# Kernel optimization log

Hardware: AMD Instinct MI355X
Metric: run time of the kernel (lower is better)

The kernel has to match this reference:

```python
import jax, jax.numpy as jnp
import numpy as np

D_MODEL = 1024
N_HEADS = 16
N_EXPERTS = 8
TOP_K = 2
EXPERT_HIDDEN = D_MODEL * 4 // N_EXPERTS  # 512, per MoELayer default


def layer_norm(x, g, b, eps=1e-5):
    mu = jnp.mean(x, axis=-1, keepdims=True)
    var = jnp.var(x, axis=-1, keepdims=True)
    return (x - mu) * jax.lax.rsqrt(var + eps) * g + b


def setup_inputs() -> dict:
    key = jax.random.key(0)
    ks = jax.random.split(key, 12)
    s = 1.0 / np.sqrt(D_MODEL)
    return {
        "x": jax.random.normal(ks[0], (2, 2048, D_MODEL), dtype=jnp.float32),
        "Wq": jax.random.normal(ks[1], (D_MODEL, D_MODEL), dtype=jnp.float32) * s,
        "Wk": jax.random.normal(ks[2], (D_MODEL, D_MODEL), dtype=jnp.float32) * s,
        "Wv": jax.random.normal(ks[3], (D_MODEL, D_MODEL), dtype=jnp.float32) * s,
        "Wo": jax.random.normal(ks[4], (D_MODEL, D_MODEL), dtype=jnp.float32) * s,
        "g1": jnp.ones((D_MODEL,), jnp.float32),
        "b1": jnp.zeros((D_MODEL,), jnp.float32),
        "g2": jnp.ones((D_MODEL,), jnp.float32),
        "b2": jnp.zeros((D_MODEL,), jnp.float32),
        "Wg": jax.random.normal(ks[5], (D_MODEL, N_EXPERTS), dtype=jnp.float32) * s,
        "W1": jax.random.normal(ks[6], (N_EXPERTS, D_MODEL, EXPERT_HIDDEN), dtype=jnp.float32) * s,
        "W2": jax.random.normal(ks[7], (N_EXPERTS, EXPERT_HIDDEN, D_MODEL), dtype=jnp.float32) * (1.0 / np.sqrt(EXPERT_HIDDEN)),
    }


def reference(x, Wq, Wk, Wv, Wo, g1, b1, g2, b2, Wg, W1, W2):
    B, S, D = x.shape
    H, dk = N_HEADS, D // N_HEADS

    # ---- pre-norm attention + residual (dropout = identity in eval) ----
    xn = layer_norm(x, g1, b1)
    q = (xn @ Wq).reshape(B, S, H, dk).transpose(0, 2, 1, 3)  # [B,H,S,dk]
    k = (xn @ Wk).reshape(B, S, H, dk).transpose(0, 2, 1, 3)
    v = (xn @ Wv).reshape(B, S, H, dk).transpose(0, 2, 1, 3)
    scores = jnp.einsum("bhqd,bhkd->bhqk", q, k) / np.sqrt(dk)
    attn = jax.nn.softmax(scores, axis=-1)
    o = jnp.einsum("bhqk,bhkd->bhqd", attn, v)
    o = o.transpose(0, 2, 1, 3).reshape(B, S, D) @ Wo
    x = x + o

    # ---- pre-norm MoE + residual ----
    xn2 = layer_norm(x, g2, b2)
    xf = xn2.reshape(B * S, D)  # [T, D]
    gate = xf @ Wg  # [T, E]
    topv, topi = jax.lax.top_k(gate, TOP_K)  # [T, K]
    probs = jax.nn.softmax(topv, axis=-1)    # softmax over top-k scores
    # dense combine weights [T, E] (top-k indices are distinct)
    cw = jnp.sum(jax.nn.one_hot(topi, N_EXPERTS, dtype=xf.dtype) * probs[..., None], axis=1)
    h = jax.nn.relu(jnp.einsum("td,edh->teh", xf, W1))  # [T,E,Hid]
    y = jnp.einsum("teh,ehd->ted", h, W2)               # [T,E,D]
    moe = jnp.einsum("ted,te->td", y, cw).reshape(B, S, D)
    return x + moe
```

## Files before the change

### kernel.cpp

```cpp
#include <hip/hip_runtime.h>

typedef __attribute__((ext_vector_type(8))) _Float16 f16x8;
typedef __attribute__((ext_vector_type(4))) _Float16 f16x4;
typedef __attribute__((ext_vector_type(8))) short bf16x8;
typedef __attribute__((ext_vector_type(4))) float f32x4;
typedef __attribute__((ext_vector_type(4))) unsigned short u16x4;
typedef __attribute__((ext_vector_type(4))) float fx4;

#define D_MODEL 1024
#define N_HEADS 16
#define SEQ 2048
#define TOKENS 4096
#define N_EXP 8
#define EHID 512
#define LO_S 2048.0f
#define INV_LO (1.0f / 2048.0f)
#define QSCALE 0.18033688011112043f
#define DTHR 11.0f

__device__ inline unsigned short f2bf(float f) {
  union { float f; unsigned u; } v; v.f = f;
  unsigned u = v.u;
  return (unsigned short)((u + 0x7FFFu + ((u >> 16) & 1u)) >> 16);
}

__device__ inline void split16(float v, _Float16& h, _Float16& l) {
  h = (_Float16)v;
  l = (_Float16)((v - (float)h) * LO_S);
}

__device__ inline void gload_lds16(const void* g, void* lds) {
  __builtin_amdgcn_global_load_lds((const __attribute__((address_space(1))) void*)g,
                                   (__attribute__((address_space(3))) void*)lds, 16, 0, 0);
}

__global__ __launch_bounds__(256) void ln_f16s_kernel(const float* __restrict__ x, const float* __restrict__ g,
                                                      const float* __restrict__ b,
                                                      _Float16* __restrict__ xh, _Float16* __restrict__ xl) {
  int t = blockIdx.x, tid = threadIdx.x;
  const float* row = x + (size_t)t * D_MODEL;
  fx4 v = *(const fx4*)(row + tid * 4);
  float s = v[0] + v[1] + v[2] + v[3];
  float s2 = v[0]*v[0] + v[1]*v[1] + v[2]*v[2] + v[3]*v[3];
  #pragma unroll
  for (int off = 1; off < 64; off <<= 1) { s += __shfl_xor(s, off); s2 += __shfl_xor(s2, off); }
  __shared__ float red[8];
  int wv = tid >> 6, wl = tid & 63;
  if (wl == 0) { red[wv] = s; red[4 + wv] = s2; }
  __syncthreads();
  s = red[0] + red[1] + red[2] + red[3];
  s2 = red[4] + red[5] + red[6] + red[7];
  float mu = s * (1.f / 1024.f);
  float var = s2 * (1.f / 1024.f) - mu * mu;
  float rstd = rsqrtf(var + 1e-5f);
  int kk = tid * 4;
  f16x4 oh, ol;
  #pragma unroll
  for (int c = 0; c < 4; c++) {
    float y = (v[c] - mu) * rstd * g[kk + c] + b[kk + c];
    _Float16 h, lo; split16(y, h, lo);
    oh[c] = h; ol[c] = lo;
  }
  *(f16x4*)(xh + (size_t)t * D_MODEL + kk) = oh;
  *(f16x4*)(xl + (size_t)t * D_MODEL + kk) = ol;
}

__global__ __launch_bounds__(256) void tcast4_kernel(const float* __restrict__ s0, const float* __restrict__ s1,
                                                     const float* __restrict__ s2, const float* __restrict__ s3,
                                                     _Float16* __restrict__ qkvh, _Float16* __restrict__ qkvl,
                                                     _Float16* __restrict__ woh, _Float16* __restrict__ wol) {
  int z = blockIdx.z;
  const float* src = (z == 0) ? s0 : (z == 1) ? s1 : (z == 2) ? s2 : s3;
  _Float16* dh = (z < 3) ? qkvh + (size_t)z * 1048576 : woh;
  _Float16* dl = (z < 3) ? qkvl + (size_t)z * 1048576 : wol;
  __shared__ float tile[32][33];
  int c0 = blockIdx.x * 32, r0 = blockIdx.y * 32;
  int tx = threadIdx.x & 31, ty = threadIdx.x >> 5;
  #pragma unroll
  for (int i = 0; i < 4; i++) tile[ty + 8*i][tx] = src[(size_t)(r0 + ty + 8*i) * 1024 + c0 + tx];
  __syncthreads();
  #pragma unroll
  for (int i = 0; i < 4; i++) {
    float v = tile[tx][ty + 8*i];
    _Float16 h, lo; split16(v, h, lo);
    size_t idx = (size_t)(c0 + ty + 8*i) * 1024 + r0 + tx;
    dh[idx] = h; dl[idx] = lo;
  }
}

__global__ __launch_bounds__(256) void tcast_bf16_kernel(const float* __restrict__ src, unsigned short* __restrict__ dst,
                                                         int R, int C) {
  __shared__ float tile[32][33];
  size_t mo = (size_t)blockIdx.z * R * C;
  src += mo; dst += mo;
  int c0 = blockIdx.x * 32, r0 = blockIdx.y * 32;
  int tx = threadIdx.x & 31, ty = threadIdx.x >> 5;
  #pragma unroll
  for (int i = 0; i < 4; i++) tile[ty + 8*i][tx] = src[(size_t)(r0 + ty + 8*i) * C + c0 + tx];
  __syncthreads();
  #pragma unroll
  for (int i = 0; i < 4; i++) dst[(size_t)(c0 + ty + 8*i) * R + r0 + tx] = f2bf(tile[tx][ty + 8*i]);
}

__device__ inline void gemm128s(const _Float16* __restrict__ Ah, const _Float16* __restrict__ Al,
                                const _Float16* __restrict__ Bh, const _Float16* __restrict__ Bl,
                                int lda, int ldb, int K, int bm, int bn,
                                _Float16* lsbuf, f32x4 (&acc)[4][4], f32x4 (&accx)[4][4]) {
  const int tid = threadIdx.x, w = tid >> 6, l = tid & 63, lr = l & 15, lg = l >> 4;
  const int wr = (w >> 1) * 64, wc = (w & 1) * 64;
  int ca = (((tid & 3) ^ ((tid >> 3) & 3)) * 8);
  int ra0 = tid >> 2, ra1 = 64 + (tid >> 2);
  const _Float16* gA0 = Ah + (size_t)(bm + ra0) * lda + ca;
  const _Float16* gA1 = Ah + (size_t)(bm + ra1) * lda + ca;
  const _Float16* gA2 = Al + (size_t)(bm + ra0) * lda + ca;
  const _Float16* gA3 = Al + (size_t)(bm + ra1) * lda + ca;
  const _Float16* gB0 = Bh + (size_t)(bn + ra0) * ldb + ca;
  const _Float16* gB1 = Bh + (size_t)(bn + ra1) * ldb + ca;
  const _Float16* gB2 = Bl + (size_t)(bn + ra0) * ldb + ca;
  const _Float16* gB3 = Bl + (size_t)(bn + ra1) * ldb + ca;
  char* base = (char*)lsbuf;
  const int wo = w * 1024;
#define STAGE8(bb, ko) do { \
    gload_lds16(gA0 + (ko), (bb) + wo);         gload_lds16(gA1 + (ko), (bb) + 4096 + wo);  \
    gload_lds16(gA2 + (ko), (bb) + 8192 + wo);  gload_lds16(gA3 + (ko), (bb) + 12288 + wo); \
    gload_lds16(gB0 + (ko), (bb) + 16384 + wo); gload_lds16(gB1 + (ko), (bb) + 20480 + wo); \
    gload_lds16(gB2 + (ko), (bb) + 24576 + wo); gload_lds16(gB3 + (ko), (bb) + 28672 + wo); } while (0)
  STAGE8(base, 0);
  __syncthreads();
  const int swzB = ((lg ^ ((lr >> 1) & 3)) << 4);
  int cur = 0;
  for (int ko = 0; ko < K; ko += 32) {
    char* bR = base + cur * 32768;
    if (ko + 32 < K) STAGE8(base + (cur ^ 1) * 32768, ko + 32);
    f16x8 ah[4], al4[4], bh4[4], bl4[4];
    #pragma unroll
    for (int m = 0; m < 4; m++) {
      int roff = (wr + m * 16 + lr) * 64 + swzB;
      ah[m]  = *(const f16x8*)(bR + roff);
      al4[m] = *(const f16x8*)(bR + 8192 + roff);
    }
    #pragma unroll
    for (int n = 0; n < 4; n++) {
      int roff = (wc + n * 16 + lr) * 64 + swzB;
      bh4[n] = *(const f16x8*)(bR + 16384 + roff);
      bl4[n] = *(const f16x8*)(bR + 24576 + roff);
    }
    __builtin_amdgcn_s_setprio(1);
    #pragma unroll
    for (int m = 0; m < 4; m++)
      #pragma unroll
      for (int n = 0; n < 4; n++) {
        acc[m][n]  = __builtin_amdgcn_mfma_f32_16x16x32_f16(ah[m], bh4[n], acc[m][n], 0, 0, 0);
        accx[m][n] = __builtin_amdgcn_mfma_f32_16x16x32_f16(ah[m], bl4[n], accx[m][n], 0, 0, 0);
        accx[m][n] = __builtin_amdgcn_mfma_f32_16x16x32_f16(al4[m], bh4[n], accx[m][n], 0, 0, 0);
      }
    __builtin_amdgcn_s_setprio(0);
    __syncthreads();
    cur ^= 1;
  }
#undef STAGE8
}

__global__ __launch_bounds__(256) void gemm_qkv_kernel(const _Float16* __restrict__ xh, const _Float16* __restrict__ xl,
                                                       const _Float16* __restrict__ Wh, const _Float16* __restrict__ Wl,
                                                       _Float16* __restrict__ qh, _Float16* __restrict__ ql,
                                                       _Float16* __restrict__ kh, _Float16* __restrict__ kl,
                                                       _Float16* __restrict__ vh, _Float16* __restrict__ vl) {
  __shared__ _Float16 ls[32768];
  f32x4 acc[4][4] = {}, accx[4][4] = {};
  int bid = blockIdx.x;
  int sw = (bid & 7) * 96 + (bid >> 3);
  int bm = (sw & 31) * 128, bn = (sw >> 5) * 128;
  gemm128s(xh, xl, Wh, Wl, 1024, 1024, 1024, bm, bn, ls, acc, accx);
  const int tid = threadIdx.x, w = tid >> 6, l = tid & 63, lr = l & 15, lg = l >> 4;
  const int wr = (w >> 1) * 64, wc = (w & 1) * 64;
  #pragma unroll
  for (int m = 0; m < 4; m++) {
    int row0 = bm + wr + m * 16 + lg * 4;
    #pragma unroll
    for (int n = 0; n < 4; n++) {
      int col = bn + wc + n * 16 + lr;
      int mat = col >> 10;
      int c = col & 1023, h = c >> 6, d = c & 63;
      if (mat == 2) {
        int bb = row0 >> 11, ss = row0 & 2047;
        int tile = ss >> 5, kvs = ss & 31;
        f16x4 ph, pl;
        #pragma unroll
        for (int j = 0; j < 4; j++) {
          float v = acc[m][n][j] + accx[m][n][j] * INV_LO;
          _Float16 hh, ll; split16(v, hh, ll);
          ph[j] = hh; pl[j] = ll;
        }
        size_t base = ((size_t)(bb * N_HEADS + h) * 64 + tile) * 2048;
        int off = d * 32 + ((((kvs >> 3) ^ ((d >> 1) & 3)) << 3) | (kvs & 7));
        *(f16x4*)(vh + base + off) = ph;
        *(f16x4*)(vl + base + off) = pl;
      } else if (mat == 1) {
        #pragma unroll
        for (int j = 0; j < 4; j++) {
          float v = acc[m][n][j] + accx[m][n][j] * INV_LO;
          _Float16 hh, ll; split16(v, hh, ll);
          int t = row0 + j, bb = t >> 11, ss = t & 2047;
          int tile = ss >> 5, r = ss & 31;
          size_t base = ((size_t)(bb * N_HEADS + h) * 64 + tile) * 2048;
          int off = r * 64 + ((((d >> 3) ^ (r & 7)) << 3) | (d & 7));
          kh[base + off] = hh; kl[base + off] = ll;
        }
      } else {
        #pragma unroll
        for (int j = 0; j < 4; j++) {
          float v = (acc[m][n][j] + accx[m][n][j] * INV_LO) * QSCALE;
          _Float16 hh, ll; split16(v, hh, ll);
          int t = row0 + j, bb = t >> 11, ss = t & 2047;
          size_t idx = ((size_t)(bb * N_HEADS + h) * SEQ + ss) * 64 + d;
          qh[idx] = hh; ql[idx] = ll;
        }
      }
    }
  }
}

__global__ __launch_bounds__(256, 4) void flash_kernel(const _Float16* __restrict__ qhp, const _Float16* __restrict__ qlp,
                                                       const _Float16* __restrict__ khs, const _Float16* __restrict__ kls,
                                                       const _Float16* __restrict__ vhs, const _Float16* __restrict__ vls,
                                                       _Float16* __restrict__ oh, _Float16* __restrict__ ol) {
  __shared__ _Float16 lsKV[2][8192];
  __shared__ _Float16 lsP[4][2][512];
  int wgid = blockIdx.x;
  int xcd = wgid & 7, kk = wgid >> 3;
  int bh = xcd * 4 + (kk >> 5), qt = kk & 31;
  int tid = threadIdx.x, w = tid >> 6, l = tid & 63, lr = l & 15, lg = l >> 4;
  int q0 = qt * 64 + w * 16;
  const _Float16* qhb = qhp + (size_t)bh * SEQ * 64;
  const _Float16* qlb = qlp + (size_t)bh * SEQ * 64;
  f16x8 qfh[2], qfl[2];
  #pragma unroll
  for (int ks = 0; ks < 2; ks++) {
    size_t idx = (size_t)(q0 + lr) * 64 + ks * 32 + lg * 8;
    qfh[ks] = *(const f16x8*)(qhb + idx);
    qfl[ks] = *(const f16x8*)(qlb + idx);
  }
  const _Float16* splane = (w == 0) ? khs : (w == 1) ? kls : (w == 2) ? vhs : vls;
  const _Float16* sbase = splane + (size_t)bh * 131072 + l * 8;

  f32x4 acc[4] = {}, accx[4] = {};
  float mst = -1e30f, lst = 0.f;

  {
    const _Float16* sp = sbase;
    _Float16* dd = &lsKV[0][w * 2048];
    gload_lds16(sp, dd); gload_lds16(sp + 512, dd + 512);
    gload_lds16(sp + 1024, dd + 1024); gload_lds16(sp + 1536, dd + 1536);
  }
  __syncthreads();

  for (int t = 0; t < 64; t++) {
    int bR = t & 1;
    if (t < 63) {
      const _Float16* sp = sbase + (size_t)(t + 1) * 2048;
      _Float16* dd = &lsKV[bR ^ 1][w * 2048];
      gload_lds16(sp, dd); gload_lds16(sp + 512, dd + 512);
      gload_lds16(sp + 1024, dd + 1024); gload_lds16(sp + 1536, dd + 1536);
    }
    char* bufB = (char*)&lsKV[bR][0];

    f32x4 s[2] = {}, sx[2] = {};
    #pragma unroll
    for (int ks = 0; ks < 2; ks++) {
      f16x8 kfh[2], kfl[2];
      #pragma unroll
      for (int m = 0; m < 2; m++) {
        int off = (m * 16 + lr) * 128 + (((ks * 4 + lg) ^ (lr & 7)) << 4);
        kfh[m] = *(const f16x8*)(bufB + off);
        kfl[m] = *(const f16x8*)(bufB + 4096 + off);
      }
      __builtin_amdgcn_s_setprio(1);
      #pragma unroll
      for (int m = 0; m < 2; m++) {
        s[m]  = __builtin_amdgcn_mfma_f32_16x16x32_f16(kfh[m], qfh[ks], s[m], 0, 0, 0);
        sx[m] = __builtin_amdgcn_mfma_f32_16x16x32_f16(kfh[m], qfl[ks], sx[m], 0, 0, 0);
        sx[m] = __builtin_amdgcn_mfma_f32_16x16x32_f16(kfl[m], qfh[ks], sx[m], 0, 0, 0);
      }
      __builtin_amdgcn_s_setprio(0);
    }

    float tm = -3e38f;
    #pragma unroll
    for (int m = 0; m < 2; m++)
      #pragma unroll
      for (int j = 0; j < 4; j++) {
        s[m][j] += sx[m][j] * INV_LO;
        tm = fmaxf(tm, s[m][j]);
      }
    tm = fmaxf(tm, __shfl_xor(tm, 16));
    tm = fmaxf(tm, __shfl_xor(tm, 32));
    if (!__all(tm - mst <= DTHR)) {
      float mnew = fmaxf(mst, tm);
      float corr = exp2f(mst - mnew);
      #pragma unroll
      for (int m2 = 0; m2 < 4; m2++)
        #pragma unroll
        for (int j = 0; j < 4; j++) { acc[m2][j] *= corr; accx[m2][j] *= corr; }
      lst *= corr;
      mst = mnew;
    }
    float psum = 0.f;
    #pragma unroll
    for (int m = 0; m < 2; m++) {
      f16x4 ph, pl;
      #pragma unroll
      for (int j = 0; j < 4; j++) {
        float p = exp2f(s[m][j] - mst);
        psum += p;
        _Float16 hh, ll; split16(p, hh, ll);
        ph[j] = hh; pl[j] = ll;
      }
      int boff = lr * 64 + ((((m * 2 + (lg >> 1)) ^ ((lr >> 1) & 3)) << 4) | ((lg & 1) * 8));
      *(f16x4*)((char*)&lsP[w][0][0] + boff) = ph;
      *(f16x4*)((char*)&lsP[w][1][0] + boff) = pl;
    }
    psum += __shfl_xor(psum, 16);
    psum += __shfl_xor(psum, 32);
    lst += psum;

    int poff = lr * 64 + ((lg ^ ((lr >> 1) & 3)) << 4);
    f16x8 pfh = *(const f16x8*)((char*)&lsP[w][0][0] + poff);
    f16x8 pfl = *(const f16x8*)((char*)&lsP[w][1][0] + poff);
    __builtin_amdgcn_s_setprio(1);
    #pragma unroll
    for (int m2 = 0; m2 < 4; m2++) {
      int voff = (m2 * 16 + lr) * 64 + ((lg ^ ((lr >> 1) & 3)) << 4);
      f16x8 vfh = *(const f16x8*)(bufB + 8192 + voff);
      f16x8 vfl = *(const f16x8*)(bufB + 12288 + voff);
      acc[m2]  = __builtin_amdgcn_mfma_f32_16x16x32_f16(vfh, pfh, acc[m2], 0, 0, 0);
      accx[m2] = __builtin_amdgcn_mfma_f32_16x16x32_f16(vfh, pfl, accx[m2], 0, 0, 0);
      accx[m2] = __builtin_amdgcn_mfma_f32_16x16x32_f16(vfl, pfh, accx[m2], 0, 0, 0);
    }
    __builtin_amdgcn_s_setprio(0);
    __syncthreads();
  }

  float inv = 1.f / lst;
  int b = bh >> 4, h = bh & 15;
  int tkn = b * SEQ + q0 + lr;
  #pragma unroll
  for (int m2 = 0; m2 < 4; m2++) {
    f16x4 ph, pl;
    #pragma unroll
    for (int j = 0; j < 4; j++) {
      float o = (acc[m2][j] + accx[m2][j] * INV_LO) * inv;
      _Float16 hh, ll; split16(o, hh, ll);
      ph[j] = hh; pl[j] = ll;
    }
    size_t idx = (size_t)tkn * D_MODEL + h * 64 + m2 * 16 + lg * 4;
    *(f16x4*)(oh + idx) = ph;
    *(f16x4*)(ol + idx) = pl;
  }
}

__global__ __launch_bounds__(256) void gemm_oproj_kernel(const _Float16* __restrict__ ah, const _Float16* __restrict__ al,
                                                         const _Float16* __restrict__ Wh, const _Float16* __restrict__ Wl,
                                                         const float* __restrict__ x, float* __restrict__ out) {
  __shared__ _Float16 ls[32768];
  f32x4 acc[4][4] = {}, accx[4][4] = {};
  int bid = blockIdx.x;
  int sw = (bid & 7) * 32 + (bid >> 3);
  int bm = (sw & 31) * 128, bn = (sw >> 5) * 128;
  gemm128s(ah, al, Wh, Wl, 1024, 1024, 1024, bm, bn, ls, acc, accx);
  const int tid = threadIdx.x, w = tid >> 6, l = tid & 63, lr = l & 15, lg = l >> 4;
  const int wr = (w >> 1) * 64, wc = (w & 1) * 64;
  #pragma unroll
  for (int m = 0; m < 4; m++) {
    int row0 = bm + wr + m * 16 + lg * 4;
    #pragma unroll
    for (int n = 0; n < 4; n++) {
      int col = bn + wc + n * 16 + lr;
      #pragma unroll
      for (int j = 0; j < 4; j++) {
        size_t idx = (size_t)(row0 + j) * D_MODEL + col;
        out[idx] = (acc[m][n][j] + accx[m][n][j] * INV_LO) + x[idx];
      }
    }
  }
}

__global__ __launch_bounds__(256) void gate_kernel(const float* __restrict__ x1, const float* __restrict__ Wg,
                                                   const float* __restrict__ g2, const float* __restrict__ b2,
                                                   unsigned short* __restrict__ xn2,
                                                   int* __restrict__ cnt, int* __restrict__ topi,
                                                   float* __restrict__ topw) {
  int t = blockIdx.x * 4 + (threadIdx.x >> 6);
  int l = threadIdx.x & 63;
  const float* row = x1 + (size_t)t * D_MODEL;
  fx4 v[4];
  float s = 0.f, s2 = 0.f;
  #pragma unroll
  for (int i = 0; i < 4; i++) {
    v[i] = *(const fx4*)(row + l * 16 + i * 4);
    #pragma unroll
    for (int c = 0; c < 4; c++) { s += v[i][c]; s2 += v[i][c] * v[i][c]; }
  }
  #pragma unroll
  for (int off = 1; off < 64; off <<= 1) { s += __shfl_xor(s, off); s2 += __shfl_xor(s2, off); }
  float mu = s * (1.f / 1024.f);
  float var = s2 * (1.f / 1024.f) - mu * mu;
  float rstd = rsqrtf(var + 1e-5f);
  float a8[8] = {0,0,0,0,0,0,0,0};
  #pragma unroll
  for (int i = 0; i < 4; i++) {
    u16x4 ox;
    #pragma unroll
    for (int c = 0; c < 4; c++) {
      int kk = l * 16 + i * 4 + c;
      float xv = (v[i][c] - mu) * rstd * g2[kk] + b2[kk];
      ox[c] = f2bf(xv);
      const float* wr_ = Wg + (size_t)kk * 8;
      fx4 wa = *(const fx4*)wr_;
      fx4 wb = *(const fx4*)(wr_ + 4);
      a8[0] += xv * wa[0]; a8[1] += xv * wa[1]; a8[2] += xv * wa[2]; a8[3] += xv * wa[3];
      a8[4] += xv * wb[0]; a8[5] += xv * wb[1]; a8[6] += xv * wb[2]; a8[7] += xv * wb[3];
    }
    *(u16x4*)(xn2 + (size_t)t * D_MODEL + l * 16 + i * 4) = ox;
  }
  #pragma unroll
  for (int e = 0; e < 8; e++)
    #pragma unroll
    for (int off = 1; off < 64; off <<= 1) a8[e] += __shfl_xor(a8[e], off);
  if (l == 0) {
    int i0 = 0; float v0 = a8[0];
    #pragma unroll
    for (int e = 1; e < 8; e++) if (a8[e] > v0) { v0 = a8[e]; i0 = e; }
    int i1 = -1; float v1 = -3.4e38f;
    #pragma unroll
    for (int e = 0; e < 8; e++) if (e != i0 && a8[e] > v1) { v1 = a8[e]; i1 = e; }
    float p0 = 1.f / (1.f + __expf(v1 - v0));
    topi[t * 2] = i0; topi[t * 2 + 1] = i1;
    topw[t * 2] = p0; topw[t * 2 + 1] = 1.f - p0;
    atomicAdd(&cnt[i0], 1); atomicAdd(&cnt[i1], 1);
  }
}

__global__ void init_kernel(int* cnt, int* perm) {
  int i = blockIdx.x * 256 + threadIdx.x;
  if (i < 8) cnt[i] = 0;
  if (i < 8448) perm[i] = 0;
}

__global__ void offsets_kernel(const int* __restrict__ cnt, int* __restrict__ poff) {
  if (threadIdx.x == 0) {
    int a = 0;
    for (int e = 0; e < 8; e++) { poff[e] = a; a += ((cnt[e] + 31) >> 5) << 5; }
  }
}

__global__ __launch_bounds__(256) void scatter_kernel(const int* __restrict__ topi,
                                                      const int* __restrict__ poff, int* __restrict__ perm,
                                                      int* __restrict__ slot_of) {
  int e = blockIdx.x, tid = threadIdx.x;
  __shared__ int basesh;
  __shared__ int wsum[4];
  if (tid == 0) basesh = poff[e];
  __syncthreads();
  for (int seg = 0; seg < 8192; seg += 256) {
    int a = seg + tid;
    int match = (topi[a] == e) ? 1 : 0;
    unsigned long long bal = __ballot(match);
    int wl = tid & 63, wv = tid >> 6;
    int lanepre = __popcll(bal & ((1ULL << wl) - 1ULL));
    if (wl == 0) wsum[wv] = __popcll(bal);
    __syncthreads();
    int wpre = 0;
    for (int i = 0; i < wv; i++) wpre += wsum[i];
    int total = wsum[0] + wsum[1] + wsum[2] + wsum[3];
    if (match) {
      int pos = basesh + wpre + lanepre;
      perm[pos] = a >> 1;
      slot_of[a] = pos;
    }
    __syncthreads();
    if (tid == 0) basesh += total;
    __syncthreads();
  }
}

__global__ __launch_bounds__(256) void moe_ffn_kernel(const unsigned short* __restrict__ xn2,
                                                      const unsigned short* __restrict__ W1T,
                                                      const unsigned short* __restrict__ W2T,
                                                      const int* __restrict__ cnt, const int* __restrict__ poff,
                                                      const int* __restrict__ perm,
                                                      float* __restrict__ y) {
  int bid = blockIdx.x;
  int e = -1, lt = bid;
  for (int i = 0; i < 8; i++) {
    int nt = (cnt[i] + 31) >> 5;
    if (lt < nt) { e = i; break; }
    lt -= nt;
  }
  if (e < 0) return;
  int slot0 = poff[e] + lt * 32;

  __shared__ int t_sh[32];
  __shared__ unsigned short lsX[32 * 32];
  __shared__ unsigned short hsh[32 * 520];
  int tid = threadIdx.x, w = tid >> 6, l = tid & 63, lr = l & 15, lg = l >> 4;
  if (tid < 32) t_sh[tid] = perm[slot0 + tid];
  __syncthreads();

  int Xr = tid >> 2;
  int Xc = (((tid & 3) ^ ((tid >> 3) & 3)) * 8);
  const unsigned short* gX = xn2 + (size_t)(tid < 128 ? t_sh[Xr & 31] : 0) * D_MODEL + Xc;
  const unsigned short* W1e = W1T + (size_t)e * EHID * D_MODEL;
  const unsigned short* W2e = W2T + (size_t)e * D_MODEL * EHID;
  const int swz = ((lg ^ ((lr >> 1) & 3)) << 3);

  f32x4 acc[2][8] = {};
  for (int ko = 0; ko < D_MODEL; ko += 32) {
    if (tid < 128) gload_lds16(gX + ko, (char*)lsX + w * 1024);
    __syncthreads();
    bf16x8 a[2];
    #pragma unroll
    for (int m = 0; m < 2; m++) a[m] = *(const bf16x8*)(lsX + (m*16 + lr) * 32 + swz);
    #pragma unroll
    for (int n = 0; n < 8; n++) {
      bf16x8 bb = *(const bf16x8*)(W1e + (size_t)(w * 128 + n * 16 + lr) * D_MODEL + ko + lg * 8);
      #pragma unroll
      for (int m = 0; m < 2; m++)
        acc[m][n] = __builtin_amdgcn_mfma_f32_16x16x32_bf16(a[m], bb, acc[m][n], 0, 0, 0);
    }
    __syncthreads();
  }
  #pragma unroll
  for (int m = 0; m < 2; m++)
    #pragma unroll
    for (int n = 0; n < 8; n++)
      #pragma unroll
      for (int j = 0; j < 4; j++)
        hsh[(m*16 + lg*4 + j) * 520 + w * 128 + n * 16 + lr] = f2bf(fmaxf(acc[m][n][j], 0.f));
  __syncthreads();

  for (int p = 0; p < 2; p++) {
    f32x4 acc2[2][8] = {};
    for (int k2 = 0; k2 < EHID; k2 += 32) {
      bf16x8 a2[2];
      #pragma unroll
      for (int m = 0; m < 2; m++) a2[m] = *(const bf16x8*)(hsh + (m*16 + lr) * 520 + k2 + lg * 8);
      #pragma unroll
      for (int n = 0; n < 8; n++) {
        int ycol = w * 256 + p * 128 + n * 16 + lr;
        bf16x8 bb = *(const bf16x8*)(W2e + (size_t)ycol * EHID + k2 + lg * 8);
        #pragma unroll
        for (int m = 0; m < 2; m++)
          acc2[m][n] = __builtin_amdgcn_mfma_f32_16x16x32_bf16(a2[m], bb, acc2[m][n], 0, 0, 0);
      }
    }
    #pragma unroll
    for (int m = 0; m < 2; m++)
      #pragma unroll
      for (int j = 0; j < 4; j++) {
        int r = m * 16 + lg * 4 + j;
        #pragma unroll
        for (int n = 0; n < 8; n++)
          y[(size_t)(slot0 + r) * D_MODEL + w * 256 + p * 128 + n * 16 + lr] = acc2[m][n][j];
      }
  }
}

__global__ __launch_bounds__(256) void combine_kernel(const float* __restrict__ y, const int* __restrict__ slot_of,
                                                      const float* __restrict__ topw, float* __restrict__ out) {
  int t = blockIdx.x * 4 + (threadIdx.x >> 6);
  int l = threadIdx.x & 63;
  int s0 = slot_of[t * 2], s1 = slot_of[t * 2 + 1];
  float w0 = topw[t * 2], w1 = topw[t * 2 + 1];
  const float* y0 = y + (size_t)s0 * D_MODEL + l * 16;
  const float* y1 = y + (size_t)s1 * D_MODEL + l * 16;
  float* o = out + (size_t)t * D_MODEL + l * 16;
  #pragma unroll
  for (int i = 0; i < 4; i++) {
    fx4 av = *(const fx4*)(y0 + i * 4);
    fx4 bv = *(const fx4*)(y1 + i * 4);
    fx4 d = *(const fx4*)(o + i * 4);
    #pragma unroll
    for (int j = 0; j < 4; j++) d[j] += w0 * av[j] + w1 * bv[j];
    *(fx4*)(o + i * 4) = d;
  }
}

#define MB (1u << 20)
extern "C" void kernel_launch(void* const* d_in, const int* in_sizes, int n_in,
                              void* d_out, int out_size, void* d_ws, size_t ws_size,
                              hipStream_t stream) {
  const float* x  = (const float*)d_in[0];
  const float* Wq = (const float*)d_in[1];
  const float* Wk = (const float*)d_in[2];
  const float* Wv = (const float*)d_in[3];
  const float* Wo = (const float*)d_in[4];
  const float* g1 = (const float*)d_in[5];
  const float* b1 = (const float*)d_in[6];
  const float* g2 = (const float*)d_in[7];
  const float* b2 = (const float*)d_in[8];
  const float* Wg = (const float*)d_in[9];
  const float* W1 = (const float*)d_in[10];
  const float* W2 = (const float*)d_in[11];
  float* out = (float*)d_out;

  char* ws = (char*)d_ws;
  _Float16* xn1h = (_Float16*)(ws + 0*MB);
  _Float16* xn1l = (_Float16*)(ws + 8*MB);
  _Float16* Wqkh = (_Float16*)(ws + 16*MB);
  _Float16* Wqkl = (_Float16*)(ws + 22*MB);
  _Float16* Woh  = (_Float16*)(ws + 28*MB);
  _Float16* Wol  = (_Float16*)(ws + 30*MB);
  _Float16* qhb  = (_Float16*)(ws + 32*MB);
  _Float16* qlb  = (_Float16*)(ws + 40*MB);
  _Float16* khb  = (_Float16*)(ws + 48*MB);
  _Float16* klb  = (_Float16*)(ws + 56*MB);
  _Float16* vhb  = (_Float16*)(ws + 64*MB);
  _Float16* vlb  = (_Float16*)(ws + 72*MB);
  unsigned short* xn2 = (unsigned short*)(ws + 80*MB);
  unsigned short* W1T = (unsigned short*)(ws + 88*MB);
  unsigned short* W2T = (unsigned short*)(ws + 96*MB);
  char* misc = ws + 104*MB;
  int*   topi    = (int*)(misc);
  float* topw    = (float*)(misc + 32768);
  int*   slot_of = (int*)(misc + 65536);
  int*   cnt     = (int*)(misc + 98304);
  int*   poff    = (int*)(misc + 98336);
  int*   perm    = (int*)(misc + 98368);
  float* ybuf    = (float*)(ws + 32*MB);
  _Float16* attnh = xn1h;
  _Float16* attnl = xn1l;

  tcast4_kernel<<<dim3(32, 32, 4), 256, 0, stream>>>(Wq, Wk, Wv, Wo, Wqkh, Wqkl, Woh, Wol);
  tcast_bf16_kernel<<<dim3(16, 32, 8), 256, 0, stream>>>(W1, W1T, 1024, 512);
  tcast_bf16_kernel<<<dim3(32, 16, 8), 256, 0, stream>>>(W2, W2T, 512, 1024);
  init_kernel<<<33, 256, 0, stream>>>(cnt, perm);

  ln_f16s_kernel<<<TOKENS, 256, 0, stream>>>(x, g1, b1, xn1h, xn1l);
  gemm_qkv_kernel<<<768, 256, 0, stream>>>(xn1h, xn1l, Wqkh, Wqkl, qhb, qlb, khb, klb, vhb, vlb);
  flash_kernel<<<1024, 256, 0, stream>>>(qhb, qlb, khb, klb, vhb, vlb, attnh, attnl);
  gemm_oproj_kernel<<<256, 256, 0, stream>>>(attnh, attnl, Woh, Wol, x, out);

  gate_kernel<<<1024, 256, 0, stream>>>(out, Wg, g2, b2, xn2, cnt, topi, topw);
  offsets_kernel<<<1, 64, 0, stream>>>(cnt, poff);
  scatter_kernel<<<8, 256, 0, stream>>>(topi, poff, perm, slot_of);
  moe_ffn_kernel<<<264, 256, 0, stream>>>(xn2, W1T, W2T, cnt, poff, perm, ybuf);
  combine_kernel<<<1024, 256, 0, stream>>>(ybuf, slot_of, topw, out);

  (void)in_sizes; (void)n_in; (void)out_size; (void)ws_size;
}
```

Measured before the change: 591.6 us.

## Fuse prep kernels, restructure MoE FFN to 64-token tiles, streamline flash softmax

Merges the four weight-cast/transpose kernels and the init kernel into one prep launch, and folds the offsets kernel into scatter and the MoE kernel, cutting launch count. The MoE FFN now works on 64-token tiles with 512 threads, chunking the hidden dimension so W1/W2 weights are reused across more tokens, with swizzled LDS staging of activations. Flash attention defers the row-max shuffles to the rescale branch, accumulates the row sum per lane and reduces it once at the end, and uses packed cvt_pkrtz for the hi/lo fp16 split. Risks are lower occupancy from the larger MoE blocks and more padding per expert, and round-toward-zero conversion of P changes precision slightly.

```diff
diff --git a/kernel.cpp b/kernel.cpp
--- a/kernel.cpp
+++ b/kernel.cpp
@@ -2,6 +2,8 @@
 
 typedef __attribute__((ext_vector_type(8))) _Float16 f16x8;
 typedef __attribute__((ext_vector_type(4))) _Float16 f16x4;
+typedef __attribute__((ext_vector_type(2))) _Float16 f16x2;
+typedef __attribute__((ext_vector_type(2))) __fp16 fp16x2_n;
 typedef __attribute__((ext_vector_type(8))) short bf16x8;
 typedef __attribute__((ext_vector_type(4))) float f32x4;
 typedef __attribute__((ext_vector_type(4))) unsigned short u16x4;
@@ -29,9 +31,71 @@
   l = (_Float16)((v - (float)h) * LO_S);
 }
 
+__device__ inline void split2(float a, float b, f16x2& h, f16x2& l) {
+  fp16x2_n hn = __builtin_amdgcn_cvt_pkrtz(a, b);
+  h = __builtin_bit_cast(f16x2, hn);
+  fp16x2_n ln = __builtin_amdgcn_cvt_pkrtz((a - (float)h[0]) * LO_S, (b - (float)h[1]) * LO_S);
+  l = __builtin_bit_cast(f16x2, ln);
+}
+
 __device__ inline void gload_lds16(const void* g, void* lds) {
   __builtin_amdgcn_global_load_lds((const __attribute__((address_space(1))) void*)g,
                                    (__attribute__((address_space(3))) void*)lds, 16, 0, 0);
+}
+
+__global__ __launch_bounds__(256) void prep_kernel(const float* __restrict__ Wq, const float* __restrict__ Wk,
+                                                   const float* __restrict__ Wv, const float* __restrict__ Wo,
+                                                   const float* __restrict__ W1, const float* __restrict__ W2,
+                                                   _Float16* __restrict__ qkvh, _Float16* __restrict__ qkvl,
+                                                   _Float16* __restrict__ woh, _Float16* __restrict__ wol,
+                                                   unsigned short* __restrict__ W1T, unsigned short* __restrict__ W2T,
+                                                   int* __restrict__ cnt, int* __restrict__ perm) {
+  int b = blockIdx.x;
+  if (b >= 12288) {
+    int i = (b - 12288) * 256 + threadIdx.x;
+    if (i < 8) cnt[i] = 0;
+    if (i < 8704) perm[i] = 0;
+    return;
+  }
+  __shared__ float tile[32][33];
+  int tx = threadIdx.x & 31, ty = threadIdx.x >> 5;
+  if (b < 4096) {
+    int z = b >> 10, rem = b & 1023;
+    int c0 = (rem & 31) * 32, r0 = (rem >> 5) * 32;
+    const float* src = (z == 0) ? Wq : (z == 1) ? Wk : (z == 2) ? Wv : Wo;
+    _Float16* dh = (z < 3) ? qkvh + (size_t)z * 1048576 : woh;
+    _Float16* dl = (z < 3) ? qkvl + (size_t)z * 1048576 : wol;
+    #pragma unroll
+    for (int i = 0; i < 4; i++) tile[ty + 8*i][tx] = src[(size_t)(r0 + ty + 8*i) * 1024 + c0 + tx];
+    __syncthreads();
+    #pragma unroll
+    for (int i = 0; i < 4; i++) {
+      float v = tile[tx][ty + 8*i];
+      _Float16 h, lo; split16(v, h, lo);
+      size_t idx = (size_t)(c0 + ty + 8*i) * 1024 + r0 + tx;
+      dh[idx] = h; dl[idx] = lo;
+    }
+  } else if (b < 8192) {
+    int q = b - 4096, z = q >> 9, rem = q & 511;
+    int c0 = (rem & 15) * 32, r0 = (rem >> 4) * 32;
+    const float* src = W1 + (size_t)z * 524288;
+    unsigned short* dst = W1T + (size_t)z * 524288;
+    #pragma unroll
+    for (int i = 0; i < 4; i++) tile[ty + 8*i][tx] = src[(size_t)(r0 + ty + 8*i) * 512 + c0 + tx];
+    __syncthreads();
+    #pragma unroll
+    for (int i = 0; i < 4; i++) dst[(size_t)(c0 + ty + 8*i) * 1024 + r0 + tx] = f2bf(tile[tx][ty + 8*i]);
+  } else {
+    int q = b - 8192, z = q >> 9, rem = q & 511;
+    int c0 = (rem & 31) * 32, r0 = (rem >> 5) * 32;
+    const float* src = W2 + (size_t)z * 524288;
+    unsigned short* dst = W2T + (size_t)z * 524288;
+    #pragma unroll
+    for (int i = 0; i < 4; i++) tile[ty + 8*i][tx] = src[(size_t)(r0 + ty + 8*i) * 1024 + c0 + tx];
+    __syncthreads();
+    #pragma unroll
+    for (int i = 0; i < 4; i++) dst[(size_t)(c0 + ty + 8*i) * 512 + r0 + tx] = f2bf(tile[tx][ty + 8*i]);
+  }
 }
 
 __global__ __launch_bounds__(256) void ln_f16s_kernel(const float* __restrict__ x, const float* __restrict__ g,
@@ -63,43 +127,6 @@
   }
   *(f16x4*)(xh + (size_t)t * D_MODEL + kk) = oh;
   *(f16x4*)(xl + (size_t)t * D_MODEL + kk) = ol;
-}
-
-__global__ __launch_bounds__(256) void tcast4_kernel(const float* __restrict__ s0, const float* __restrict__ s1,
-                                                     const float* __restrict__ s2, const float* __restrict__ s3,
-                                                     _Float16* __restrict__ qkvh, _Float16* __restrict__ qkvl,
-                                                     _Float16* __restrict__ woh, _Float16* __restrict__ wol) {
-  int z = blockIdx.z;
-  const float* src = (z == 0) ? s0 : (z == 1) ? s1 : (z == 2) ? s2 : s3;
-  _Float16* dh = (z < 3) ? qkvh + (size_t)z * 1048576 : woh;
-  _Float16* dl = (z < 3) ? qkvl + (size_t)z * 1048576 : wol;
-  __shared__ float tile[32][33];
-  int c0 = blockIdx.x * 32, r0 = blockIdx.y * 32;
-  int tx = threadIdx.x & 31, ty = threadIdx.x >> 5;
-  #pragma unroll
-  for (int i = 0; i < 4; i++) tile[ty + 8*i][tx] = src[(size_t)(r0 + ty + 8*i) * 1024 + c0 + tx];
-  __syncthreads();
-  #pragma unroll
-  for (int i = 0; i < 4; i++) {
-    float v = tile[tx][ty + 8*i];
-    _Float16 h, lo; split16(v, h, lo);
-    size_t idx = (size_t)(c0 + ty + 8*i) * 1024 + r0 + tx;
-    dh[idx] = h; dl[idx] = lo;
-  }
-}
-
-__global__ __launch_bounds__(256) void tcast_bf16_kernel(const float* __restrict__ src, unsigned short* __restrict__ dst,
-                                                         int R, int C) {
-  __shared__ float tile[32][33];
-  size_t mo = (size_t)blockIdx.z * R * C;
-  src += mo; dst += mo;
-  int c0 = blockIdx.x * 32, r0 = blockIdx.y * 32;
-  int tx = threadIdx.x & 31, ty = threadIdx.x >> 5;
-  #pragma unroll
-  for (int i = 0; i < 4; i++) tile[ty + 8*i][tx] = src[(size_t)(r0 + ty + 8*i) * C + c0 + tx];
-  __syncthreads();
-  #pragma unroll
-  for (int i = 0; i < 4; i++) dst[(size_t)(c0 + ty + 8*i) * R + r0 + tx] = f2bf(tile[tx][ty + 8*i]);
 }
 
 __device__ inline void gemm128s(const _Float16* __restrict__ Ah, const _Float16* __restrict__ Al,
@@ -245,7 +272,7 @@
   const _Float16* sbase = splane + (size_t)bh * 131072 + l * 8;
 
   f32x4 acc[4] = {}, accx[4] = {};
-  float mst = -1e30f, lst = 0.f;
+  float mst = -1e30f, lstp = 0.f;
 
   {
     const _Float16* sp = sbase;
@@ -293,36 +320,36 @@
         s[m][j] += sx[m][j] * INV_LO;
         tm = fmaxf(tm, s[m][j]);
       }
-    tm = fmaxf(tm, __shfl_xor(tm, 16));
-    tm = fmaxf(tm, __shfl_xor(tm, 32));
     if (!__all(tm - mst <= DTHR)) {
+      tm = fmaxf(tm, __shfl_xor(tm, 16));
+      tm = fmaxf(tm, __shfl_xor(tm, 32));
       float mnew = fmaxf(mst, tm);
       float corr = exp2f(mst - mnew);
       #pragma unroll
       for (int m2 = 0; m2 < 4; m2++)
         #pragma unroll
         for (int j = 0; j < 4; j++) { acc[m2][j] *= corr; accx[m2][j] *= corr; }
-      lst *= corr;
+      lstp *= corr;
       mst = mnew;
     }
-    float psum = 0.f;
     #pragma unroll
     for (int m = 0; m < 2; m++) {
-      f16x4 ph, pl;
       #pragma unroll
       for (int j = 0; j < 4; j++) {
         float p = exp2f(s[m][j] - mst);
-        psum += p;
-        _Float16 hh, ll; split16(p, hh, ll);
-        ph[j] = hh; pl[j] = ll;
-      }
+        lstp += p;
+        s[m][j] = p;
+      }
+      f16x2 h01, h23, l01, l23;
+      split2(s[m][0], s[m][1], h01, l01);
+      split2(s[m][2], s[m][3], h23, l23);
+      f16x4 ph, pl;
+      ph[0] = h01[0]; ph[1] = h01[1]; ph[2] = h23[0]; ph[3] = h23[1];
+      pl[0] = l01[0]; pl[1] = l01[1]; pl[2] = l23[0]; pl[3] = l23[1];
       int boff = lr * 64 + ((((m * 2 + (lg >> 1)) ^ ((lr >> 1) & 3)) << 4) | ((lg & 1) * 8));
       *(f16x4*)((char*)&lsP[w][0][0] + boff) = ph;
       *(f16x4*)((char*)&lsP[w][1][0] + boff) = pl;
     }
-    psum += __shfl_xor(psum, 16);
-    psum += __shfl_xor(psum, 32);
-    lst += psum;
 
     int poff = lr * 64 + ((lg ^ ((lr >> 1) & 3)) << 4);
     f16x8 pfh = *(const f16x8*)((char*)&lsP[w][0][0] + poff);
@@ -341,6 +368,8 @@
     __syncthreads();
   }
 
+  float lst = lstp + __shfl_xor(lstp, 16);
+  lst += __shfl_xor(lst, 32);
   float inv = 1.f / lst;
   int b = bh >> 4, h = bh & 15;
   int tkn = b * SEQ + q0 + lr;
@@ -441,26 +470,16 @@
   }
 }
 
-__global__ void init_kernel(int* cnt, int* perm) {
-  int i = blockIdx.x * 256 + threadIdx.x;
-  if (i < 8) cnt[i] = 0;
-  if (i < 8448) perm[i] = 0;
-}
-
-__global__ void offsets_kernel(const int* __restrict__ cnt, int* __restrict__ poff) {
-  if (threadIdx.x == 0) {
-    int a = 0;
-    for (int e = 0; e < 8; e++) { poff[e] = a; a += ((cnt[e] + 31) >> 5) << 5; }
-  }
-}
-
-__global__ __launch_bounds__(256) void scatter_kernel(const int* __restrict__ topi,
-                                                      const int* __restrict__ poff, int* __restrict__ perm,
-                                                      int* __restrict__ slot_of) {
+__global__ __launch_bounds__(256) void scatter_kernel(const int* __restrict__ topi, const int* __restrict__ cnt,
+                                                      int* __restrict__ perm, int* __restrict__ slot_of) {
   int e = blockIdx.x, tid = threadIdx.x;
   __shared__ int basesh;
   __shared__ int wsum[4];
-  if (tid == 0) basesh = poff[e];
+  if (tid == 0) {
+    int a = 0;
+    for (int i = 0; i < e; i++) a += ((cnt[i] + 63) >> 6) << 6;
+    basesh = a;
+  }
   __syncthreads();
   for (int seg = 0; seg < 8192; seg += 256) {
     int a = seg + tid;
@@ -484,86 +503,96 @@
   }
 }
 
-__global__ __launch_bounds__(256) void moe_ffn_kernel(const unsigned short* __restrict__ xn2,
+__global__ __launch_bounds__(512) void moe_ffn_kernel(const unsigned short* __restrict__ xn2,
                                                       const unsigned short* __restrict__ W1T,
                                                       const unsigned short* __restrict__ W2T,
-                                                      const int* __restrict__ cnt, const int* __restrict__ poff,
+                                                      const int* __restrict__ cnt,
                                                       const int* __restrict__ perm,
                                                       float* __restrict__ y) {
   int bid = blockIdx.x;
-  int e = -1, lt = bid;
+  int e = -1, lt = bid, off = 0;
   for (int i = 0; i < 8; i++) {
-    int nt = (cnt[i] + 31) >> 5;
+    int nt = (cnt[i] + 63) >> 6;
     if (lt < nt) { e = i; break; }
-    lt -= nt;
+    lt -= nt; off += nt << 6;
   }
   if (e < 0) return;
-  int slot0 = poff[e] + lt * 32;
-
-  __shared__ int t_sh[32];
-  __shared__ unsigned short lsX[32 * 32];
-  __shared__ unsigned short hsh[32 * 520];
+  int slot0 = off + lt * 64;
+
+  __shared__ int t_sh[64];
+  __shared__ unsigned short lsX[64 * 128];
+  __shared__ unsigned short hsh[64 * 264];
   int tid = threadIdx.x, w = tid >> 6, l = tid & 63, lr = l & 15, lg = l >> 4;
-  if (tid < 32) t_sh[tid] = perm[slot0 + tid];
+  if (tid < 64) t_sh[tid] = perm[slot0 + tid];
   __syncthreads();
 
-  int Xr = tid >> 2;
-  int Xc = (((tid & 3) ^ ((tid >> 3) & 3)) * 8);
-  const unsigned short* gX = xn2 + (size_t)(tid < 128 ? t_sh[Xr & 31] : 0) * D_MODEL + Xc;
   const unsigned short* W1e = W1T + (size_t)e * EHID * D_MODEL;
   const unsigned short* W2e = W2T + (size_t)e * D_MODEL * EHID;
-  const int swz = ((lg ^ ((lr >> 1) & 3)) << 3);
-
-  f32x4 acc[2][8] = {};
-  for (int ko = 0; ko < D_MODEL; ko += 32) {
-    if (tid < 128) gload_lds16(gX + ko, (char*)lsX + w * 1024);
-    __syncthreads();
-    bf16x8 a[2];
-    #pragma unroll
-    for (int m = 0; m < 2; m++) a[m] = *(const bf16x8*)(lsX + (m*16 + lr) * 32 + swz);
-    #pragma unroll
-    for (int n = 0; n < 8; n++) {
-      bf16x8 bb = *(const bf16x8*)(W1e + (size_t)(w * 128 + n * 16 + lr) * D_MODEL + ko + lg * 8);
-      #pragma unroll
-      for (int m = 0; m < 2; m++)
-        acc[m][n] = __builtin_amdgcn_mfma_f32_16x16x32_bf16(a[m], bb, acc[m][n], 0, 0, 0);
-    }
-    __syncthreads();
-  }
-  #pragma unroll
-  for (int m = 0; m < 2; m++)
-    #pragma unroll
-    for (int n = 0; n < 8; n++)
-      #pragma unroll
-      for (int j = 0; j < 4; j++)
-        hsh[(m*16 + lg*4 + j) * 520 + w * 128 + n * 16 + lr] = f2bf(fmaxf(acc[m][n][j], 0.f));
-  __syncthreads();
-
-  for (int p = 0; p < 2; p++) {
-    f32x4 acc2[2][8] = {};
-    for (int k2 = 0; k2 < EHID; k2 += 32) {
-      bf16x8 a2[2];
-      #pragma unroll
-      for (int m = 0; m < 2; m++) a2[m] = *(const bf16x8*)(hsh + (m*16 + lr) * 520 + k2 + lg * 8);
+
+  f32x4 acc2[4][8] = {};
+  for (int h = 0; h < 2; h++) {
+    f32x4 acc1[4][2] = {};
+    for (int kc = 0; kc < 8; kc++) {
+      __syncthreads();
+      #pragma unroll
+      for (int L = 0; L < 2; L++) {
+        int u = tid + 512 * L;
+        int r = u >> 4, sp = u & 15;
+        int cs = (sp & 8) | ((sp & 7) ^ (r & 7));
+        gload_lds16(xn2 + (size_t)t_sh[r] * D_MODEL + kc * 128 + cs * 8, (char*)lsX + u * 16);
+      }
+      __syncthreads();
+      #pragma unroll
+      for (int kst = 0; kst < 4; kst++) {
+        bf16x8 a[4];
+        #pragma unroll
+        for (int m = 0; m < 4; m++) {
+          int row = m * 16 + lr;
+          int slot = kst * 4 + lg;
+          int cs = (slot & 8) | ((slot & 7) ^ (row & 7));
+          a[m] = *(const bf16x8*)((char*)lsX + row * 256 + cs * 16);
+        }
+        int ko = kc * 128 + kst * 32;
+        #pragma unroll
+        for (int n = 0; n < 2; n++) {
+          bf16x8 bb = *(const bf16x8*)(W1e + (size_t)(h * 256 + w * 32 + n * 16 + lr) * D_MODEL + ko + lg * 8);
+          #pragma unroll
+          for (int m = 0; m < 4; m++)
+            acc1[m][n] = __builtin_amdgcn_mfma_f32_16x16x32_bf16(a[m], bb, acc1[m][n], 0, 0, 0);
+        }
+      }
+    }
+    __syncthreads();
+    #pragma unroll
+    for (int m = 0; m < 4; m++)
+      #pragma unroll
+      for (int n = 0; n < 2; n++)
+        #pragma unroll
+        for (int j = 0; j < 4; j++)
+          hsh[(m*16 + lg*4 + j) * 264 + w * 32 + n * 16 + lr] = f2bf(fmaxf(acc1[m][n][j], 0.f));
+    __syncthreads();
+    for (int k2 = 0; k2 < 256; k2 += 32) {
+      bf16x8 a2[4];
+      #pragma unroll
+      for (int m = 0; m < 4; m++) a2[m] = *(const bf16x8*)(hsh + (m*16 + lr) * 264 + k2 + lg * 8);
       #pragma unroll
       for (int n = 0; n < 8; n++) {
-        int ycol = w * 256 + p * 128 + n * 16 + lr;
-        bf16x8 bb = *(const bf16x8*)(W2e + (size_t)ycol * EHID + k2 + lg * 8);
-        #pragma unroll
-        for (int m = 0; m < 2; m++)
+        bf16x8 bb = *(const bf16x8*)(W2e + (size_t)(w * 128 + n * 16 + lr) * EHID + h * 256 + k2 + lg * 8);
+        #pragma unroll
+        for (int m = 0; m < 4; m++)
           acc2[m][n] = __builtin_amdgcn_mfma_f32_16x16x32_bf16(a2[m], bb, acc2[m][n], 0, 0, 0);
       }
     }
-    #pragma unroll
-    for (int m = 0; m < 2; m++)
-      #pragma unroll
-      for (int j = 0; j < 4; j++) {
-        int r = m * 16 + lg * 4 + j;
-        #pragma unroll
-        for (int n = 0; n < 8; n++)
-          y[(size_t)(slot0 + r) * D_MODEL + w * 256 + p * 128 + n * 16 + lr] = acc2[m][n][j];
-      }
-  }
+  }
+  #pragma unroll
+  for (int m = 0; m < 4; m++)
+    #pragma unroll
+    for (int j = 0; j < 4; j++) {
+      int r = m * 16 + lg * 4 + j;
+      #pragma unroll
+      for (int n = 0; n < 8; n++)
+        y[(size_t)(slot0 + r) * D_MODEL + w * 128 + n * 16 + lr] = acc2[m][n][j];
+    }
 }
 
 __global__ __launch_bounds__(256) void combine_kernel(const float* __restrict__ y, const int* __restrict__ slot_of,
@@ -625,16 +654,12 @@
   float* topw    = (float*)(misc + 32768);
   int*   slot_of = (int*)(misc + 65536);
   int*   cnt     = (int*)(misc + 98304);
-  int*   poff    = (int*)(misc + 98336);
   int*   perm    = (int*)(misc + 98368);
   float* ybuf    = (float*)(ws + 32*MB);
   _Float16* attnh = xn1h;
   _Float16* attnl = xn1l;
 
-  tcast4_kernel<<<dim3(32, 32, 4), 256, 0, stream>>>(Wq, Wk, Wv, Wo, Wqkh, Wqkl, Woh, Wol);
-  tcast_bf16_kernel<<<dim3(16, 32, 8), 256, 0, stream>>>(W1, W1T, 1024, 512);
-  tcast_bf16_kernel<<<dim3(32, 16, 8), 256, 0, stream>>>(W2, W2T, 512, 1024);
-  init_kernel<<<33, 256, 0, stream>>>(cnt, perm);
+  prep_kernel<<<12322, 256, 0, stream>>>(Wq, Wk, Wv, Wo, W1, W2, Wqkh, Wqkl, Woh, Wol, W1T, W2T, cnt, perm);
 
   ln_f16s_kernel<<<TOKENS, 256, 0, stream>>>(x, g1, b1, xn1h, xn1l);
   gemm_qkv_kernel<<<768, 256, 0, stream>>>(xn1h, xn1l, Wqkh, Wqkl, qhb, qlb, khb, klb, vhb, vlb);
@@ -642,9 +667,8 @@
   gemm_oproj_kernel<<<256, 256, 0, stream>>>(attnh, attnl, Woh, Wol, x, out);
 
   gate_kernel<<<1024, 256, 0, stream>>>(out, Wg, g2, b2, xn2, cnt, topi, topw);
-  offsets_kernel<<<1, 64, 0, stream>>>(cnt, poff);
-  scatter_kernel<<<8, 256, 0, stream>>>(topi, poff, perm, slot_of);
-  moe_ffn_kernel<<<264, 256, 0, stream>>>(xn2, W1T, W2T, cnt, poff, perm, ybuf);
+  scatter_kernel<<<8, 256, 0, stream>>>(topi, cnt, perm, slot_of);
+  moe_ffn_kernel<<<136, 512, 0, stream>>>(xn2, W1T, W2T, cnt, perm, ybuf);
   combine_kernel<<<1024, 256, 0, stream>>>(ybuf, slot_of, topw, out);
 
   (void)in_sizes; (void)n_in; (void)out_size; (void)ws_size;
```

Result: faster. 529.7 us (-10.5%).
